# Kernel tuning notes

Hardware: AMD Instinct MI355X
Metric: run time of the kernel (lower is better)

## Reference

```python
import jax, jax.numpy as jnp
import numpy as np

EPS_RHO = 1e-8
EPS_DEN = 1e-9


def _rho_signed_sqrt(x):
    return jnp.sqrt(jax.nn.relu(x) + EPS_RHO) - jnp.sqrt(jax.nn.relu(-x) + EPS_RHO)


def setup_inputs() -> dict:
    key = jax.random.key(0)
    ks = jax.random.split(key, 8)
    B, N, C, A = 2, 512, 1024, 64  # batch, seq, hidden_dim, attn_dim
    s_c = 1.0 / np.sqrt(C)
    s_a = 1.0 / np.sqrt(A)
    return {
        "X": jax.random.normal(ks[0], (B, N, C), jnp.float32),
        "Wq": jax.random.normal(ks[1], (A, C), jnp.float32) * s_c,   # Linear(C->A), no bias
        "Wk": jax.random.normal(ks[2], (A, C), jnp.float32) * s_c,   # Linear(C->A), no bias
        "Wphi": jax.random.normal(ks[3], (A,), jnp.float32) * s_a,   # Linear(A->1), no bias
        "Wy_w": jax.random.normal(ks[4], (C, C), jnp.float32) * s_c, # Linear(C->C)
        "Wy_b": jax.random.normal(ks[5], (C,), jnp.float32) * s_c,
        "We_w": jax.random.normal(ks[6], (C, A), jnp.float32) * s_a, # Linear(A->C)
        "We_b": jax.random.normal(ks[7], (C,), jnp.float32) * s_a,
    }


def reference(X, Wq, Wk, Wphi, Wy_w, Wy_b, We_w, We_b):
    # q, k: (B,N,A); Vy: (B,N,C)
    q = jnp.einsum('bnc,ac->bna', X, Wq)
    k = jnp.einsum('bnc,ac->bna', X, Wk)
    Vy = jnp.einsum('bnc,dc->bnd', X, Wy_w) + Wy_b

    # pairwise features e_ij = relu(rho(q_i + k_j)): (B,N,N,A)
    e = jax.nn.relu(_rho_signed_sqrt(q[:, :, None, :] + k[:, None, :, :]))

    # scores: (B,N,N); stable exp with per-row max (== online-softmax result)
    scores = jnp.einsum('bija,a->bij', e, Wphi)
    m = jnp.max(scores, axis=-1, keepdims=True)
    ex = jnp.exp(scores - m)
    denom = jnp.sum(ex, axis=-1)  # (B,N)

    # part1 = exp_scores @ Vy
    part1 = jnp.einsum('bij,bjc->bic', ex, Vy)
    # part2 = sum_j ex_ij * (We e_ij + be) = We(sum_j ex_ij e_ij) + be * denom  (We is linear)
    Ew = jnp.einsum('bij,bija->bia', ex, e)  # (B,N,A)
    part2 = jnp.einsum('bia,ca->bic', Ew, We_w) + We_b * denom[..., None]

    return (part1 + part2) / (denom[..., None] + EPS_DEN)
```

## Files before the change

kernel.cpp:

```cpp
#include <hip/hip_runtime.h>
#include <math.h>

#define EPS_RHO 1e-8f
#define EPS_DEN 1e-9f

constexpr int Bb = 2;
constexpr int Nn = 512;
constexpr int Cc = 1024;
constexpr int Aa = 64;
constexpr int TOK = Bb * Nn;
constexpr int KG  = 640;

typedef __attribute__((ext_vector_type(8))) short short8;
typedef __attribute__((ext_vector_type(4))) short short4v;
typedef __attribute__((ext_vector_type(4))) float f32x4;

__device__ __forceinline__ float e_fn(float s) {
    const float SQE = 9.9999994e-05f;
    return sqrtf(fmaxf(s, 0.f) + EPS_RHO) - SQE;
}

__device__ __forceinline__ short f2bf(float x) {
    union { float f; unsigned u; } v; v.f = x;
    unsigned r = v.u + 0x7FFFu + ((v.u >> 16) & 1u);
    return (short)(r >> 16);
}

__device__ __forceinline__ unsigned cvt_pk_bf16(float e0, float e1) {
    unsigned d;
    asm("v_cvt_pk_bf16_f32 %0, %1, %2" : "=v"(d) : "v"(e0), "v"(e1));
    return d;
}

constexpr int PREP_N0 = 1024 * 1024;
constexpr int PREP_N1 = 1152 * 1024;
constexpr int PREP_N2 = 2 * 1024 * 128;
constexpr int PREP_TOT = PREP_N0 + PREP_N1 + PREP_N2;

__global__ __launch_bounds__(256) void prep_kernel(
    const float* __restrict__ X, const float* __restrict__ Wy_w,
    const float* __restrict__ Wq, const float* __restrict__ Wk,
    const float* __restrict__ We_w,
    short* __restrict__ Xb, short* __restrict__ Wb, short* __restrict__ Gt)
{
    int g = (blockIdx.x * 256 + threadIdx.x) * 4;
    if (g >= PREP_TOT) return;

    if (g < PREP_N0 + PREP_N1) {
        const float* src;
        short* dst;
        if (g < PREP_N0) { src = X + g; dst = Xb + g; }
        else {
            int i2 = g - PREP_N0;
            if (i2 < 1048576)       src = Wy_w + i2;
            else if (i2 < 1114112)  src = Wq + (i2 - 1048576);
            else                    src = Wk + (i2 - 1114112);
            dst = Wb + i2;
        }
        float4 v = *(const float4*)src;
        short4v o = { f2bf(v.x), f2bf(v.y), f2bf(v.z), f2bf(v.w) };
        *(short4v*)dst = o;
    } else {
        int i3 = g - PREP_N0 - PREP_N1;
        int b = i3 >> 17;
        int r = i3 & 131071;
        int c = r >> 7, s = r & 127;
        short4v o = {0, 0, 0, 0};
        if (s < 64) {
            float4 v = *(const float4*)(We_w + (size_t)c * Aa + s);
            o.x = f2bf(v.x); o.y = f2bf(v.y); o.z = f2bf(v.z); o.w = f2bf(v.w);
        }
        *(short4v*)(Gt + ((size_t)(b * 1024 + c)) * KG + 512 + s) = o;
    }
}

__global__ __launch_bounds__(256) void gemm_mega_direct(
    const short* __restrict__ Xb,
    const short* __restrict__ Wb,
    const float* __restrict__ Wy_b,
    short* __restrict__ Gt,
    float* __restrict__ qg,
    float* __restrict__ kTg)
{
    constexpr int K = 1024;
    int tid = threadIdx.x, wid = tid >> 6, lane = tid & 63;
    int bm = blockIdx.y * 32, bn = blockIdx.x * 32;
    int fr = lane & 15, fk = (lane >> 4) * 8;

    const short* A0 = Xb + (size_t)(bm + fr) * K + wid * 256 + fk;
    const short* B0 = Wb + (size_t)(bn + fr) * K + wid * 256 + fk;

    f32x4 acc[2][2] = {};
    #pragma unroll 4
    for (int s = 0; s < 8; ++s) {
        short8 a0 = *(const short8*)(A0 + s * 32);
        short8 a1 = *(const short8*)(A0 + 16 * K + s * 32);
        short8 b0 = *(const short8*)(B0 + s * 32);
        short8 b1 = *(const short8*)(B0 + 16 * K + s * 32);
        acc[0][0] = __builtin_amdgcn_mfma_f32_16x16x32_bf16(a0, b0, acc[0][0], 0, 0, 0);
        acc[0][1] = __builtin_amdgcn_mfma_f32_16x16x32_bf16(a0, b1, acc[0][1], 0, 0, 0);
        acc[1][0] = __builtin_amdgcn_mfma_f32_16x16x32_bf16(a1, b0, acc[1][0], 0, 0, 0);
        acc[1][1] = __builtin_amdgcn_mfma_f32_16x16x32_bf16(a1, b1, acc[1][1], 0, 0, 0);
    }

    __shared__ float red[4][32][34];
    int cr = (lane >> 4) * 4, cc = lane & 15;
    #pragma unroll
    for (int mi = 0; mi < 2; ++mi)
        #pragma unroll
        for (int ni = 0; ni < 2; ++ni)
            #pragma unroll
            for (int r_ = 0; r_ < 4; ++r_)
                red[wid][mi * 16 + cr + r_][ni * 16 + cc] = acc[mi][ni][r_];
    __syncthreads();

    int r = tid >> 3, c0 = (tid & 7) * 4;
    int m = bm + r;
    int bsel = m >> 9, j = m & 511;
    #pragma unroll
    for (int u = 0; u < 4; ++u) {
        int n = bn + c0 + u;
        float sum = red[0][r][c0 + u] + red[1][r][c0 + u]
                  + red[2][r][c0 + u] + red[3][r][c0 + u];
        if (n < 1024) {
            Gt[((size_t)(bsel * 1024 + n)) * KG + j] = f2bf(sum + Wy_b[n]);
        } else if (n < 1088) {
            qg[(size_t)m * Aa + (n - 1024)] = sum;
        } else {
            kTg[((size_t)(bsel * 64 + (n - 1088))) * 512 + j] = sum;
        }
    }
}

__global__ __launch_bounds__(256) void attn1_fused(
    const float* __restrict__ qg,
    const float* __restrict__ kTg,
    const float* __restrict__ Wphi,
    short* __restrict__ P,
    float* __restrict__ denomg)
{
    __shared__ __align__(16) float qs[Aa];
    __shared__ __align__(16) float wph[Aa];
    __shared__ __align__(16) short E[256][72];
    __shared__ __align__(16) float exs[256];
    __shared__ __align__(16) float red[256];
    __shared__ __align__(16) float ewp[8][Aa];

    int t = blockIdx.x;
    int b = t >> 9;
    int tid = threadIdx.x;

    if (tid < Aa) {
        qs[tid] = qg[(size_t)t * Aa + tid];
        wph[tid] = Wphi[tid];
    }
    __syncthreads();

    const float* kT = kTg + (size_t)b * Aa * 512;

    float dsum = 0.f;
    float ew0 = 0.f, ew1 = 0.f;
    int pa2 = (tid & 31) * 2;
    int pg8 = tid >> 5;

    #pragma unroll
    for (int c = 0; c < 2; ++c) {
        int j = c * 256 + tid;

        float s = 0.f;
        #pragma unroll
        for (int a0 = 0; a0 < Aa; a0 += 8) {
            float e[8];
            #pragma unroll
            for (int u = 0; u < 8; ++u) {
                float kv = kT[(size_t)(a0 + u) * 512 + j];
                e[u] = e_fn(qs[a0 + u] + kv);
                s += wph[a0 + u] * e[u];
            }
            uint4 pk;
            pk.x = cvt_pk_bf16(e[0], e[1]);
            pk.y = cvt_pk_bf16(e[2], e[3]);
            pk.z = cvt_pk_bf16(e[4], e[5]);
            pk.w = cvt_pk_bf16(e[6], e[7]);
            *(uint4*)&E[tid][a0] = pk;
        }
        float ex = expf(s);
        exs[tid] = ex;
        dsum += ex;
        P[(size_t)t * KG + j] = f2bf(ex);
        __syncthreads();

        #pragma unroll 8
        for (int jj = 0; jj < 32; ++jj) {
            int jr = pg8 * 32 + jj;
            unsigned ue = *(const unsigned*)&E[jr][pa2];
            float e0 = __uint_as_float(ue << 16);
            float e1 = __uint_as_float(ue & 0xFFFF0000u);
            float x = exs[jr];
            ew0 += x * e0;
            ew1 += x * e1;
        }
        __syncthreads();
    }

    red[tid] = dsum;
    __syncthreads();
    for (int off = 128; off > 0; off >>= 1) {
        if (tid < off) red[tid] += red[tid + off];
        __syncthreads();
    }
    if (tid == 0) denomg[t] = red[0];

    ewp[pg8][pa2] = ew0;
    ewp[pg8][pa2 + 1] = ew1;
    __syncthreads();
    if (tid < Aa) {
        float ew = 0.f;
        #pragma unroll
        for (int g = 0; g < 8; ++g) ew += ewp[g][tid];
        P[(size_t)t * KG + 512 + tid] = f2bf(ew);
    } else if (tid < 128) {
        P[(size_t)t * KG + 576 + (tid - 64)] = 0;
    }
}

__global__ __launch_bounds__(256) void gemm_attn2_direct(
    const short* __restrict__ P,
    const short* __restrict__ Gt,
    const float* __restrict__ We_b,
    const float* __restrict__ denomg,
    float* __restrict__ out)
{
    int tid = threadIdx.x, wid = tid >> 6, lane = tid & 63;
    int bm = blockIdx.y * 32, bn = blockIdx.x * 32;
    int bsel = bm >> 9;
    int fr = lane & 15, fk = (lane >> 4) * 8;

    const short* A0 = P + (size_t)(bm + fr) * KG + wid * 160 + fk;
    const short* B0 = Gt + ((size_t)(bsel * 1024) + bn + fr) * KG + wid * 160 + fk;

    f32x4 acc[2][2] = {};
    #pragma unroll
    for (int s = 0; s < 5; ++s) {
        short8 a0 = *(const short8*)(A0 + s * 32);
        short8 a1 = *(const short8*)(A0 + (size_t)16 * KG + s * 32);
        short8 b0 = *(const short8*)(B0 + s * 32);
        short8 b1 = *(const short8*)(B0 + (size_t)16 * KG + s * 32);
        acc[0][0] = __builtin_amdgcn_mfma_f32_16x16x32_bf16(a0, b0, acc[0][0], 0, 0, 0);
        acc[0][1] = __builtin_amdgcn_mfma_f32_16x16x32_bf16(a0, b1, acc[0][1], 0, 0, 0);
        acc[1][0] = __builtin_amdgcn_mfma_f32_16x16x32_bf16(a1, b0, acc[1][0], 0, 0, 0);
        acc[1][1] = __builtin_amdgcn_mfma_f32_16x16x32_bf16(a1, b1, acc[1][1], 0, 0, 0);
    }

    __shared__ float red[4][32][34];
    int cr = (lane >> 4) * 4, cc = lane & 15;
    #pragma unroll
    for (int mi = 0; mi < 2; ++mi)
        #pragma unroll
        for (int ni = 0; ni < 2; ++ni)
            #pragma unroll
            for (int r_ = 0; r_ < 4; ++r_)
                red[wid][mi * 16 + cr + r_][ni * 16 + cc] = acc[mi][ni][r_];
    __syncthreads();

    int r = tid >> 3, c0 = (tid & 7) * 4;
    int m = bm + r;
    float dn = denomg[m];
    float inv = 1.f / (dn + EPS_DEN);
    float4 o;
    float* op = &o.x;
    #pragma unroll
    for (int u = 0; u < 4; ++u) {
        int n = bn + c0 + u;
        float sum = red[0][r][c0 + u] + red[1][r][c0 + u]
                  + red[2][r][c0 + u] + red[3][r][c0 + u];
        op[u] = (sum + We_b[n] * dn) * inv;
    }
    *(float4*)(out + (size_t)m * Cc + bn + c0) = o;
}

extern "C" void kernel_launch(void* const* d_in, const int* in_sizes, int n_in,
                              void* d_out, int out_size, void* d_ws, size_t ws_size,
                              hipStream_t stream)
{
    const float* X    = (const float*)d_in[0];
    const float* Wq   = (const float*)d_in[1];
    const float* Wk   = (const float*)d_in[2];
    const float* Wphi = (const float*)d_in[3];
    const float* Wy_w = (const float*)d_in[4];
    const float* Wy_b = (const float*)d_in[5];
    const float* We_w = (const float*)d_in[6];
    const float* We_b = (const float*)d_in[7];
    float* out = (float*)d_out;

    float* ws = (float*)d_ws;
    float* qg     = ws;
    float* kTg    = qg + (size_t)TOK * Aa;
    float* denomg = kTg + (size_t)TOK * Aa;
    short* Xb     = (short*)(denomg + 1024);
    short* Wb     = Xb + (size_t)1024 * 1024;
    short* Gt     = Wb + (size_t)1152 * 1024;
    short* P      = Gt + (size_t)2 * 1024 * KG;

    prep_kernel<<<(PREP_TOT / 4 + 255) / 256, 256, 0, stream>>>(
        X, Wy_w, Wq, Wk, We_w, Xb, Wb, Gt);

    dim3 gg(36, 32);
    gemm_mega_direct<<<gg, 256, 0, stream>>>(Xb, Wb, Wy_b, Gt, qg, kTg);

    attn1_fused<<<TOK, 256, 0, stream>>>(qg, kTg, Wphi, P, denomg);

    dim3 g2(32, 32);
    gemm_attn2_direct<<<g2, 256, 0, stream>>>(P, Gt, We_b, denomg, out);
}
```

Measured before the change: 135.8 us.

## Make attn1 wave-local to drop block barriers and use shuffle reductions

Each wavefront of the attention kernel now owns a contiguous 128-key slice. It keeps its own LDS tile of pairwise features and exp scores, so the weighted feature sum only needs an lgkmcnt wait instead of block-wide __syncthreads. Each lane accumulates one feature column with two interleaved FMA chains. The denominator reduction becomes a wave shuffle followed by a 4-way combine, replacing the shared-memory tree of barriers. Zeroing of the padding columns of P moves into the prep kernel, which adds a small amount of extra prep work in exchange for a shorter attention tail.

```diff
diff --git a/kernel.cpp b/kernel.cpp
--- a/kernel.cpp
+++ b/kernel.cpp
@@ -35,13 +35,15 @@
 constexpr int PREP_N0 = 1024 * 1024;
 constexpr int PREP_N1 = 1152 * 1024;
 constexpr int PREP_N2 = 2 * 1024 * 128;
-constexpr int PREP_TOT = PREP_N0 + PREP_N1 + PREP_N2;
+constexpr int PREP_N3 = 1024 * 64;
+constexpr int PREP_TOT = PREP_N0 + PREP_N1 + PREP_N2 + PREP_N3;
 
 __global__ __launch_bounds__(256) void prep_kernel(
     const float* __restrict__ X, const float* __restrict__ Wy_w,
     const float* __restrict__ Wq, const float* __restrict__ Wk,
     const float* __restrict__ We_w,
-    short* __restrict__ Xb, short* __restrict__ Wb, short* __restrict__ Gt)
+    short* __restrict__ Xb, short* __restrict__ Wb, short* __restrict__ Gt,
+    short* __restrict__ P)
 {
     int g = (blockIdx.x * 256 + threadIdx.x) * 4;
     if (g >= PREP_TOT) return;
@@ -60,7 +62,7 @@
         float4 v = *(const float4*)src;
         short4v o = { f2bf(v.x), f2bf(v.y), f2bf(v.z), f2bf(v.w) };
         *(short4v*)dst = o;
-    } else {
+    } else if (g < PREP_N0 + PREP_N1 + PREP_N2) {
         int i3 = g - PREP_N0 - PREP_N1;
         int b = i3 >> 17;
         int r = i3 & 131071;
@@ -71,6 +73,11 @@
             o.x = f2bf(v.x); o.y = f2bf(v.y); o.z = f2bf(v.z); o.w = f2bf(v.w);
         }
         *(short4v*)(Gt + ((size_t)(b * 1024 + c)) * KG + 512 + s) = o;
+    } else {
+        int i4 = g - PREP_N0 - PREP_N1 - PREP_N2;
+        int t = i4 >> 6, s = i4 & 63;
+        short4v o = {0, 0, 0, 0};
+        *(short4v*)(P + (size_t)t * KG + 576 + s) = o;
     }
 }
 
@@ -132,23 +139,24 @@
     }
 }
 
-__global__ __launch_bounds__(256) void attn1_fused(
+__global__ __launch_bounds__(256) void attn1_wave(
     const float* __restrict__ qg,
     const float* __restrict__ kTg,
     const float* __restrict__ Wphi,
     short* __restrict__ P,
     float* __restrict__ denomg)
 {
+    __shared__ __align__(16) short E[4][64][72];
+    __shared__ __align__(16) float exs[4][64];
     __shared__ __align__(16) float qs[Aa];
     __shared__ __align__(16) float wph[Aa];
-    __shared__ __align__(16) short E[256][72];
-    __shared__ __align__(16) float exs[256];
-    __shared__ __align__(16) float red[256];
-    __shared__ __align__(16) float ewp[8][Aa];
+    __shared__ __align__(16) float ewp[4][Aa];
+    __shared__ float dred[4];
 
     int t = blockIdx.x;
     int b = t >> 9;
     int tid = threadIdx.x;
+    int w = tid >> 6, lane = tid & 63;
 
     if (tid < Aa) {
         qs[tid] = qg[(size_t)t * Aa + tid];
@@ -160,12 +168,10 @@
 
     float dsum = 0.f;
     float ew0 = 0.f, ew1 = 0.f;
-    int pa2 = (tid & 31) * 2;
-    int pg8 = tid >> 5;
 
     #pragma unroll
     for (int c = 0; c < 2; ++c) {
-        int j = c * 256 + tid;
+        int j = w * 128 + c * 64 + lane;
 
         float s = 0.f;
         #pragma unroll
@@ -175,53 +181,46 @@
             for (int u = 0; u < 8; ++u) {
                 float kv = kT[(size_t)(a0 + u) * 512 + j];
                 e[u] = e_fn(qs[a0 + u] + kv);
-                s += wph[a0 + u] * e[u];
+                s = fmaf(wph[a0 + u], e[u], s);
             }
             uint4 pk;
             pk.x = cvt_pk_bf16(e[0], e[1]);
             pk.y = cvt_pk_bf16(e[2], e[3]);
             pk.z = cvt_pk_bf16(e[4], e[5]);
             pk.w = cvt_pk_bf16(e[6], e[7]);
-            *(uint4*)&E[tid][a0] = pk;
+            *(uint4*)&E[w][lane][a0] = pk;
         }
         float ex = expf(s);
-        exs[tid] = ex;
+        exs[w][lane] = ex;
         dsum += ex;
         P[(size_t)t * KG + j] = f2bf(ex);
-        __syncthreads();
+
+        asm volatile("s_waitcnt lgkmcnt(0)" ::: "memory");
+        __builtin_amdgcn_sched_barrier(0);
 
         #pragma unroll 8
-        for (int jj = 0; jj < 32; ++jj) {
-            int jr = pg8 * 32 + jj;
-            unsigned ue = *(const unsigned*)&E[jr][pa2];
-            float e0 = __uint_as_float(ue << 16);
-            float e1 = __uint_as_float(ue & 0xFFFF0000u);
-            float x = exs[jr];
-            ew0 += x * e0;
-            ew1 += x * e1;
-        }
-        __syncthreads();
-    }
-
-    red[tid] = dsum;
+        for (int jj = 0; jj < 64; jj += 2) {
+            float x0 = exs[w][jj];
+            float x1 = exs[w][jj + 1];
+            unsigned u0 = (unsigned)(unsigned short)E[w][jj][lane];
+            unsigned u1 = (unsigned)(unsigned short)E[w][jj + 1][lane];
+            ew0 = fmaf(x0, __uint_as_float(u0 << 16), ew0);
+            ew1 = fmaf(x1, __uint_as_float(u1 << 16), ew1);
+        }
+        __builtin_amdgcn_sched_barrier(0);
+    }
+
+    ewp[w][lane] = ew0 + ew1;
+    #pragma unroll
+    for (int m_ = 1; m_ < 64; m_ <<= 1) dsum += __shfl_xor(dsum, m_, 64);
+    if (lane == 0) dred[w] = dsum;
     __syncthreads();
-    for (int off = 128; off > 0; off >>= 1) {
-        if (tid < off) red[tid] += red[tid + off];
-        __syncthreads();
-    }
-    if (tid == 0) denomg[t] = red[0];
-
-    ewp[pg8][pa2] = ew0;
-    ewp[pg8][pa2 + 1] = ew1;
-    __syncthreads();
+
     if (tid < Aa) {
-        float ew = 0.f;
-        #pragma unroll
-        for (int g = 0; g < 8; ++g) ew += ewp[g][tid];
+        float ew = ewp[0][tid] + ewp[1][tid] + ewp[2][tid] + ewp[3][tid];
         P[(size_t)t * KG + 512 + tid] = f2bf(ew);
-    } else if (tid < 128) {
-        P[(size_t)t * KG + 576 + (tid - 64)] = 0;
-    }
+    }
+    if (tid == 0) denomg[t] = dred[0] + dred[1] + dred[2] + dred[3];
 }
 
 __global__ __launch_bounds__(256) void gemm_attn2_direct(
@@ -303,12 +302,12 @@
     short* P      = Gt + (size_t)2 * 1024 * KG;
 
     prep_kernel<<<(PREP_TOT / 4 + 255) / 256, 256, 0, stream>>>(
-        X, Wy_w, Wq, Wk, We_w, Xb, Wb, Gt);
+        X, Wy_w, Wq, Wk, We_w, Xb, Wb, Gt, P);
 
     dim3 gg(36, 32);
     gemm_mega_direct<<<gg, 256, 0, stream>>>(Xb, Wb, Wy_b, Gt, qg, kTg);
 
-    attn1_fused<<<TOK, 256, 0, stream>>>(qg, kTg, Wphi, P, denomg);
+    attn1_wave<<<TOK, 256, 0, stream>>>(qg, kTg, Wphi, P, denomg);
 
     dim3 g2(32, 32);
     gemm_attn2_direct<<<g2, 256, 0, stream>>>(P, Gt, We_b, denomg, out);
```

After: 131.0 us. -3.6%, faster.
